# Kernel optimization log

Measured on AMD Instinct MI355X. Metric: run time of the kernel, lower is better.

Reference implementation:

```python
import jax, jax.numpy as jnp
import numpy as np

N = 50000      # nodes
E = 300000     # edges
IN = 128       # input_dim
HID = 64       # hidden_dim (per-head out_channels)
HEADS = 4
OUT = 64       # output_dim


def setup_inputs() -> dict:
    key = jax.random.key(0)
    ks = jax.random.split(key, 12)
    s_in = 1.0 / np.sqrt(IN)
    s_h = 1.0 / np.sqrt(HID)
    x = jax.random.normal(ks[0], (N, IN), jnp.float32)
    edge_index = jax.random.randint(ks[1], (2, E), 0, N, jnp.int32)
    Wq = jax.random.normal(ks[2], (IN, HEADS * HID), jnp.float32) * s_in
    bq = jax.random.normal(ks[3], (HEADS * HID,), jnp.float32) * 0.01
    Wk = jax.random.normal(ks[4], (IN, HEADS * HID), jnp.float32) * s_in
    bk = jax.random.normal(ks[5], (HEADS * HID,), jnp.float32) * 0.01
    Wv = jax.random.normal(ks[6], (IN, HEADS * HID), jnp.float32) * s_in
    bv = jax.random.normal(ks[7], (HEADS * HID,), jnp.float32) * 0.01
    Wskip = jax.random.normal(ks[8], (IN, HID), jnp.float32) * s_in
    bskip = jax.random.normal(ks[9], (HID,), jnp.float32) * 0.01
    Wmlp = jax.random.normal(ks[10], (HID, OUT), jnp.float32) * s_h  # spectral-normed, bias=False
    return {"x": x, "edge_index": edge_index, "Wq": Wq, "bq": bq, "Wk": Wk,
            "bk": bk, "Wv": Wv, "bv": bv, "Wskip": Wskip, "bskip": bskip,
            "Wmlp": Wmlp}


def _spectral_sigma(W, n_iter=20):
    # Power iteration as in torch spectral_norm; u,v detached, sigma = u^T W v.
    u = jnp.ones((W.shape[0],), W.dtype)
    u = u / jnp.linalg.norm(u)
    v = None
    for _ in range(n_iter):
        v = W.T @ u
        v = v / (jnp.linalg.norm(v) + 1e-12)
        u = W @ v
        u = u / (jnp.linalg.norm(u) + 1e-12)
    u = jax.lax.stop_gradient(u)
    v = jax.lax.stop_gradient(v)
    return u @ (W @ v)


def reference(x, edge_index, Wq, bq, Wk, bk, Wv, bv, Wskip, bskip, Wmlp):
    n = x.shape[0]
    src, dst = edge_index[0], edge_index[1]  # message flows src -> dst
    q = (x @ Wq + bq).reshape(n, HEADS, HID)
    k = (x @ Wk + bk).reshape(n, HEADS, HID)
    v = (x @ Wv + bv).reshape(n, HEADS, HID)
    # per-edge attention logits: [E, H]
    alpha = jnp.einsum('ehd,ehd->eh', q[dst], k[src]) / jnp.sqrt(jnp.float32(HID))
    # segment softmax over incoming edges of each dst node
    m = jax.ops.segment_max(alpha, dst, num_segments=n)          # [N, H]
    ex = jnp.exp(alpha - m[dst])                                  # [E, H]
    denom = jax.ops.segment_sum(ex, dst, num_segments=n)         # [N, H]
    a = ex / (denom[dst] + 1e-16)                                 # [E, H]
    msg = a[:, :, None] * v[src]                                  # [E, H, D]
    out = jax.ops.segment_sum(msg, dst, num_segments=n)          # [N, H, D]
    out = out.mean(axis=1) + x @ Wskip + bskip                    # concat=False -> head mean; root skip
    hidden = jnp.tanh(out)
    sigma = _spectral_sigma(Wmlp)
    return hidden @ (Wmlp / sigma)
```

## Files before the change

kernel.cpp:

```cpp
#include <hip/hip_runtime.h>
#include <math.h>

#define NN 50000
#define NE 300000
#define IND 128
#define QKV 256
#define QKVP 768
#define OUTD 64
#define NTOT 832
#define NCT 13
#define SCAN_B 196

typedef __attribute__((ext_vector_type(8))) short bf16x8;
typedef __attribute__((ext_vector_type(4))) float f32x4;

__device__ inline unsigned short f2bf(float f) {
    unsigned u = __float_as_uint(f);
    u = (u + 0x7FFFu + ((u >> 16) & 1u)) >> 16;
    return (unsigned short)u;
}
__device__ inline float b2f(unsigned short h) {
    return __uint_as_float(((unsigned)h) << 16);
}

__global__ __launch_bounds__(256) void pack_w(const float* __restrict__ Wq, const float* __restrict__ bq,
                                              const float* __restrict__ Wk, const float* __restrict__ bk,
                                              const float* __restrict__ Wv, const float* __restrict__ bv,
                                              const float* __restrict__ Wsk, const float* __restrict__ bsk,
                                              unsigned short* __restrict__ WT, float* __restrict__ bias) {
    int t = blockIdx.x * 256 + threadIdx.x;
    if (t >= NTOT * 128) return;
    int col = t >> 7, kk = t & 127;
    const float* W; const float* B; int c; int ld;
    if (col < 256)      { W = Wq;  B = bq;  c = col;       ld = 256; }
    else if (col < 512) { W = Wk;  B = bk;  c = col - 256; ld = 256; }
    else if (col < 768) { W = Wv;  B = bv;  c = col - 512; ld = 256; }
    else                { W = Wsk; B = bsk; c = col - 768; ld = 64;  }
    WT[t] = f2bf(W[kk * ld + c]);
    if (kk == 0) bias[col] = B[c];
}

__global__ __launch_bounds__(256) void gemm_mfma(const float* __restrict__ x,
                                                 const unsigned short* __restrict__ WT,
                                                 const float* __restrict__ bias,
                                                 unsigned short* __restrict__ qkvh,
                                                 float* __restrict__ skip) {
    __shared__ short As[64][136];
    __shared__ short Bs[64][136];
    int tid = threadIdx.x;
    int wv = tid >> 6, lane = tid & 63;
    int row0 = blockIdx.x * 64;

#pragma unroll
    for (int p = 0; p < 8; p++) {
        int idx = p * 256 + tid;
        int r = idx >> 5, c4 = (idx & 31) * 4;
        int gr = row0 + r;
        float4 v = (gr < NN) ? *(const float4*)(x + (size_t)gr * IND + c4)
                             : make_float4(0.f, 0.f, 0.f, 0.f);
        ushort4 o;
        o.x = f2bf(v.x); o.y = f2bf(v.y); o.z = f2bf(v.z); o.w = f2bf(v.w);
        *(ushort4*)(&As[r][c4]) = o;
    }

    int lr = lane & 15;
    int koff = (lane >> 4) * 8;
    int arow = wv * 16 + lr;
    int rbase = wv * 16 + ((lane >> 4) << 2);

    for (int ct = 0; ct < NCT; ct++) {
        int col0 = ct * 64;
        __syncthreads();
#pragma unroll
        for (int rr = 0; rr < 4; rr++) {
            int idx = rr * 256 + tid;
            int r = idx >> 4, c8 = (idx & 15) * 8;
            *(int4*)(&Bs[r][c8]) = *(const int4*)(WT + (size_t)(col0 + r) * 128 + c8);
        }
        __syncthreads();

        f32x4 acc[4] = {};
#pragma unroll
        for (int k0 = 0; k0 < 128; k0 += 32) {
            bf16x8 a = *(bf16x8*)(&As[arow][k0 + koff]);
#pragma unroll
            for (int cf = 0; cf < 4; cf++) {
                bf16x8 b = *(bf16x8*)(&Bs[cf * 16 + lr][k0 + koff]);
                acc[cf] = __builtin_amdgcn_mfma_f32_16x16x32_bf16(a, b, acc[cf], 0, 0, 0);
            }
        }

        if (col0 < QKVP) {
#pragma unroll
            for (int cf = 0; cf < 4; cf++) {
                int c = col0 + cf * 16 + lr; float bb = bias[c];
#pragma unroll
                for (int r = 0; r < 4; r++) {
                    int gr = row0 + rbase + r;
                    if (gr < NN) qkvh[(size_t)gr * QKVP + c] = f2bf(acc[cf][r] + bb);
                }
            }
        } else {
#pragma unroll
            for (int cf = 0; cf < 4; cf++) {
                int c = col0 + cf * 16 + lr; float bb = bias[c];
#pragma unroll
                for (int r = 0; r < 4; r++) {
                    int gr = row0 + rbase + r;
                    if (gr < NN) skip[(size_t)gr * OUTD + (c - QKVP)] = acc[cf][r] + bb;
                }
            }
        }
    }
}

__global__ void hist_dst(const int* __restrict__ ei, int* __restrict__ deg) {
    int t = blockIdx.x * blockDim.x + threadIdx.x;
    if (t < NE) atomicAdd(&deg[ei[NE + t]], 1);
}
__global__ __launch_bounds__(256) void scan1(const int* __restrict__ deg,
                                             int* __restrict__ incl, int* __restrict__ bsum) {
    __shared__ int s[256];
    int tid = threadIdx.x, i = blockIdx.x * 256 + tid;
    int v = (i < NN) ? deg[i] : 0;
    s[tid] = v; __syncthreads();
    for (int off = 1; off < 256; off <<= 1) {
        int t2 = (tid >= off) ? s[tid - off] : 0;
        __syncthreads(); s[tid] += t2; __syncthreads();
    }
    if (i < NN) incl[i] = s[tid];
    if (tid == 255) bsum[blockIdx.x] = s[255];
}
__global__ __launch_bounds__(256) void scan2(int* __restrict__ bsum, int* __restrict__ row_ptr) {
    __shared__ int s[256];
    int tid = threadIdx.x;
    int v = (tid < SCAN_B) ? bsum[tid] : 0;
    s[tid] = v; __syncthreads();
    for (int off = 1; off < 256; off <<= 1) {
        int t2 = (tid >= off) ? s[tid - off] : 0;
        __syncthreads(); s[tid] += t2; __syncthreads();
    }
    if (tid < SCAN_B) bsum[tid] = s[tid] - v;
    if (tid == 255) row_ptr[NN] = s[255];
}
__global__ __launch_bounds__(256) void scan3(const int* __restrict__ deg, const int* __restrict__ incl,
                                             const int* __restrict__ bsum,
                                             int* __restrict__ row_ptr, int* __restrict__ cursor) {
    int i = blockIdx.x * 256 + threadIdx.x;
    if (i < NN) {
        int e = incl[i] - deg[i] + bsum[blockIdx.x];
        row_ptr[i] = e; cursor[i] = e;
    }
}
__global__ void fill_csr(const int* __restrict__ ei, int* __restrict__ cursor,
                         int* __restrict__ col_src) {
    int t = blockIdx.x * blockDim.x + threadIdx.x;
    if (t < NE) {
        int pos = atomicAdd(&cursor[ei[NE + t]], 1);
        col_src[pos] = ei[t];
    }
}

__global__ __launch_bounds__(256) void fused_attn(const int* __restrict__ row_ptr,
                                                  const int* __restrict__ col_src,
                                                  const unsigned short* __restrict__ qkvh,
                                                  float* __restrict__ agg) {
    int wv = threadIdx.x >> 6;
    int lane = threadIdx.x & 63;
    int n = blockIdx.x * 4 + wv;
    if (n >= NN) return;

    ushort4 qq = *(const ushort4*)(qkvh + (size_t)n * QKVP + lane * 4);
    float4 qv = make_float4(b2f(qq.x), b2f(qq.y), b2f(qq.z), b2f(qq.w));
    float m = -1e30f, d = 0.f;
    float4 o = make_float4(0.f, 0.f, 0.f, 0.f);

    int jb = row_ptr[n], je = row_ptr[n + 1];
    for (int j = jb; j < je; j++) {
        int src = col_src[j];
        const unsigned short* srow = qkvh + (size_t)src * QKVP;
        ushort4 kq = *(const ushort4*)(srow + 256 + lane * 4);
        float s = qv.x * b2f(kq.x) + qv.y * b2f(kq.y) + qv.z * b2f(kq.z) + qv.w * b2f(kq.w);
        s += __shfl_xor(s, 1);
        s += __shfl_xor(s, 2);
        s += __shfl_xor(s, 4);
        s += __shfl_xor(s, 8);
        s *= 0.125f;
        float mn = fmaxf(m, s);
        float scale = __expf(m - mn);
        float e = __expf(s - mn);
        d = d * scale + e;
        ushort4 vq = *(const ushort4*)(srow + 512 + lane * 4);
        o.x = o.x * scale + e * b2f(vq.x);
        o.y = o.y * scale + e * b2f(vq.y);
        o.z = o.z * scale + e * b2f(vq.z);
        o.w = o.w * scale + e * b2f(vq.w);
        m = mn;
    }
    float inv = 1.0f / (d + 1e-16f);
    *(float4*)(agg + (size_t)n * QKV + lane * 4) =
        make_float4(o.x * inv, o.y * inv, o.z * inv, o.w * inv);
}

__global__ void spectral(const float* __restrict__ W, float* __restrict__ sigma) {
    __shared__ float ub[64], vb[64];
    int t = threadIdx.x;
    ub[t] = 0.125f;
    __syncthreads();
    for (int it = 0; it < 20; it++) {
        float s = 0.f;
        for (int i = 0; i < 64; i++) s += W[i * 64 + t] * ub[i];
        float ss = s * s;
        for (int off = 1; off < 64; off <<= 1) ss += __shfl_xor(ss, off);
        float vn = s / (sqrtf(ss) + 1e-12f);
        __syncthreads();
        vb[t] = vn;
        __syncthreads();
        float s2 = 0.f;
        for (int j = 0; j < 64; j++) s2 += W[t * 64 + j] * vb[j];
        float ss2 = s2 * s2;
        for (int off = 1; off < 64; off <<= 1) ss2 += __shfl_xor(ss2, off);
        ub[t] = s2 / (sqrtf(ss2) + 1e-12f);
        __syncthreads();
    }
    float wvv = 0.f;
    for (int j = 0; j < 64; j++) wvv += W[t * 64 + j] * vb[j];
    float sg = ub[t] * wvv;
    for (int off = 1; off < 64; off <<= 1) sg += __shfl_xor(sg, off);
    if (t == 0) *sigma = sg;
}

__global__ __launch_bounds__(256) void finalize(const float* __restrict__ agg,
                                                const float* __restrict__ skip,
                                                const float* __restrict__ Wmlp,
                                                const float* __restrict__ sigma,
                                                float* __restrict__ out) {
    __shared__ float Ws[64 * 64];
    __shared__ float hid[4][64];
    int tid = threadIdx.x;
    for (int i = tid; i < 64 * 64; i += 256) Ws[i] = Wmlp[i];
    float inv_sigma = 1.0f / (*sigma);
    __syncthreads();
    int wave = tid >> 6, lane = tid & 63;
    int n = blockIdx.x * 4 + wave;
    if (n < NN) {
        const float* a = agg + (size_t)n * QKV;
        float mval = 0.25f * (a[lane] + a[64 + lane] + a[128 + lane] + a[192 + lane])
                     + skip[(size_t)n * 64 + lane];
        hid[wave][lane] = tanhf(mval);
    }
    __syncthreads();
    if (n < NN) {
        float acc = 0.f;
        for (int d = 0; d < 64; d++) acc += hid[wave][d] * Ws[d * 64 + lane];
        out[(size_t)n * 64 + lane] = acc * inv_sigma;
    }
}

extern "C" void kernel_launch(void* const* d_in, const int* in_sizes, int n_in,
                              void* d_out, int out_size, void* d_ws, size_t ws_size,
                              hipStream_t stream) {
    const float* x     = (const float*)d_in[0];
    const int*   ei    = (const int*)d_in[1];
    const float* Wq    = (const float*)d_in[2];
    const float* bq    = (const float*)d_in[3];
    const float* Wk    = (const float*)d_in[4];
    const float* bk    = (const float*)d_in[5];
    const float* Wv    = (const float*)d_in[6];
    const float* bv    = (const float*)d_in[7];
    const float* Wskip = (const float*)d_in[8];
    const float* bskip = (const float*)d_in[9];
    const float* Wmlp  = (const float*)d_in[10];
    float* out = (float*)d_out;

    float* agg  = (float*)d_ws;
    float* skip = agg  + (size_t)NN * QKV;
    float* bias = skip + (size_t)NN * OUTD;
    float* sig  = bias + NTOT;
    int* deg     = (int*)(sig + 4);
    int* incl    = deg + NN;
    int* row_ptr = incl + NN;
    int* cursor  = row_ptr + NN + 4;
    int* col_src = cursor + NN;
    int* bsum    = col_src + NE;
    unsigned short* qkvh = (unsigned short*)(bsum + 256);
    unsigned short* WT   = qkvh + (size_t)NN * QKVP;

    hipLaunchKernelGGL(spectral, dim3(1), dim3(64), 0, stream, Wmlp, sig);

    hipMemsetAsync(deg, 0, NN * sizeof(int), stream);
    hipLaunchKernelGGL(hist_dst, dim3((NE + 255) / 256), dim3(256), 0, stream, ei, deg);
    hipLaunchKernelGGL(scan1, dim3(SCAN_B), dim3(256), 0, stream, deg, incl, bsum);
    hipLaunchKernelGGL(scan2, dim3(1), dim3(256), 0, stream, bsum, row_ptr);
    hipLaunchKernelGGL(scan3, dim3(SCAN_B), dim3(256), 0, stream, deg, incl, bsum, row_ptr, cursor);
    hipLaunchKernelGGL(fill_csr, dim3((NE + 255) / 256), dim3(256), 0, stream, ei, cursor, col_src);

    hipLaunchKernelGGL(pack_w, dim3((NTOT * 128 + 255) / 256), dim3(256), 0, stream,
                       Wq, bq, Wk, bk, Wv, bv, Wskip, bskip, WT, bias);

    hipLaunchKernelGGL(gemm_mfma, dim3((NN + 63) / 64), dim3(256), 0, stream,
                       x, WT, bias, qkvh, skip);

    hipLaunchKernelGGL(fused_attn, dim3((NN + 3) / 4), dim3(256), 0, stream,
                       row_ptr, col_src, qkvh, agg);

    hipLaunchKernelGGL(finalize, dim3((NN + 3) / 4), dim3(256), 0, stream,
                       agg, skip, Wmlp, sig, out);
}
```

Baseline: 318.4 us.

## Fuse finalize into attention, unroll edge loop, widen GEMM row tile

Merges the finalize stage (head mean, skip add, tanh, MLP projection) into the attention kernel, so the per-node aggregate buffer is never written to or read back from global memory. The edge loop now handles two edges per iteration with independent online-softmax states, merged at the end, to expose more memory-level parallelism on the gathers. The GEMM tile grows to 128 rows per block so each B tile load is reused twice. The spectral-norm loops are split into four partial accumulators. Costs are extra LDS and register use per block, and the Wmlp load now runs in every attention block.

```diff
diff --git a/kernel.cpp b/kernel.cpp
--- a/kernel.cpp
+++ b/kernel.cpp
@@ -45,14 +45,14 @@
                                                  const float* __restrict__ bias,
                                                  unsigned short* __restrict__ qkvh,
                                                  float* __restrict__ skip) {
-    __shared__ short As[64][136];
+    __shared__ short As[128][136];
     __shared__ short Bs[64][136];
     int tid = threadIdx.x;
     int wv = tid >> 6, lane = tid & 63;
-    int row0 = blockIdx.x * 64;
-
-#pragma unroll
-    for (int p = 0; p < 8; p++) {
+    int row0 = blockIdx.x * 128;
+
+#pragma unroll
+    for (int p = 0; p < 16; p++) {
         int idx = p * 256 + tid;
         int r = idx >> 5, c4 = (idx & 31) * 4;
         int gr = row0 + r;
@@ -65,8 +65,9 @@
 
     int lr = lane & 15;
     int koff = (lane >> 4) * 8;
-    int arow = wv * 16 + lr;
-    int rbase = wv * 16 + ((lane >> 4) << 2);
+    int arow0 = wv * 16 + lr;
+    int arow1 = 64 + arow0;
+    int rb = wv * 16 + ((lane >> 4) << 2);
 
     for (int ct = 0; ct < NCT; ct++) {
         int col0 = ct * 64;
@@ -79,35 +80,43 @@
         }
         __syncthreads();
 
-        f32x4 acc[4] = {};
+        f32x4 accA[4] = {}, accB[4] = {};
 #pragma unroll
         for (int k0 = 0; k0 < 128; k0 += 32) {
-            bf16x8 a = *(bf16x8*)(&As[arow][k0 + koff]);
+            bf16x8 a0 = *(bf16x8*)(&As[arow0][k0 + koff]);
+            bf16x8 a1 = *(bf16x8*)(&As[arow1][k0 + koff]);
 #pragma unroll
             for (int cf = 0; cf < 4; cf++) {
                 bf16x8 b = *(bf16x8*)(&Bs[cf * 16 + lr][k0 + koff]);
-                acc[cf] = __builtin_amdgcn_mfma_f32_16x16x32_bf16(a, b, acc[cf], 0, 0, 0);
+                accA[cf] = __builtin_amdgcn_mfma_f32_16x16x32_bf16(a0, b, accA[cf], 0, 0, 0);
+                accB[cf] = __builtin_amdgcn_mfma_f32_16x16x32_bf16(a1, b, accB[cf], 0, 0, 0);
             }
         }
 
-        if (col0 < QKVP) {
-#pragma unroll
-            for (int cf = 0; cf < 4; cf++) {
-                int c = col0 + cf * 16 + lr; float bb = bias[c];
-#pragma unroll
-                for (int r = 0; r < 4; r++) {
-                    int gr = row0 + rbase + r;
-                    if (gr < NN) qkvh[(size_t)gr * QKVP + c] = f2bf(acc[cf][r] + bb);
+#pragma unroll
+        for (int strip = 0; strip < 2; strip++) {
+            int gr0 = row0 + strip * 64 + rb;
+            if (col0 < QKVP) {
+#pragma unroll
+                for (int cf = 0; cf < 4; cf++) {
+                    int c = col0 + cf * 16 + lr; float bb = bias[c];
+                    f32x4 av = strip ? accB[cf] : accA[cf];
+#pragma unroll
+                    for (int r = 0; r < 4; r++) {
+                        int gr = gr0 + r;
+                        if (gr < NN) qkvh[(size_t)gr * QKVP + c] = f2bf(av[r] + bb);
+                    }
                 }
-            }
-        } else {
-#pragma unroll
-            for (int cf = 0; cf < 4; cf++) {
-                int c = col0 + cf * 16 + lr; float bb = bias[c];
-#pragma unroll
-                for (int r = 0; r < 4; r++) {
-                    int gr = row0 + rbase + r;
-                    if (gr < NN) skip[(size_t)gr * OUTD + (c - QKVP)] = acc[cf][r] + bb;
+            } else {
+#pragma unroll
+                for (int cf = 0; cf < 4; cf++) {
+                    int c = col0 + cf * 16 + lr; float bb = bias[c];
+                    f32x4 av = strip ? accB[cf] : accA[cf];
+#pragma unroll
+                    for (int r = 0; r < 4; r++) {
+                        int gr = gr0 + r;
+                        if (gr < NN) skip[(size_t)gr * OUTD + (c - QKVP)] = av[r] + bb;
+                    }
                 }
             }
         }
@@ -164,42 +173,107 @@
 __global__ __launch_bounds__(256) void fused_attn(const int* __restrict__ row_ptr,
                                                   const int* __restrict__ col_src,
                                                   const unsigned short* __restrict__ qkvh,
-                                                  float* __restrict__ agg) {
-    int wv = threadIdx.x >> 6;
-    int lane = threadIdx.x & 63;
+                                                  const float* __restrict__ skipb,
+                                                  const float* __restrict__ Wmlp,
+                                                  const float* __restrict__ sigma,
+                                                  float* __restrict__ out) {
+    __shared__ float Ws[64 * 64];
+    __shared__ float hid[4][64];
+    int tid = threadIdx.x;
+    for (int i = tid; i < 64 * 64; i += 256) Ws[i] = Wmlp[i];
+    float inv_sigma = 1.0f / (*sigma);
+    __syncthreads();
+
+    int wv = tid >> 6;
+    int lane = tid & 63;
     int n = blockIdx.x * 4 + wv;
-    if (n >= NN) return;
 
     ushort4 qq = *(const ushort4*)(qkvh + (size_t)n * QKVP + lane * 4);
     float4 qv = make_float4(b2f(qq.x), b2f(qq.y), b2f(qq.z), b2f(qq.w));
-    float m = -1e30f, d = 0.f;
-    float4 o = make_float4(0.f, 0.f, 0.f, 0.f);
+
+    float m0 = -1e30f, d0 = 0.f;
+    float4 o0 = make_float4(0.f, 0.f, 0.f, 0.f);
+    float m1 = -1e30f, d1 = 0.f;
+    float4 o1 = make_float4(0.f, 0.f, 0.f, 0.f);
 
     int jb = row_ptr[n], je = row_ptr[n + 1];
-    for (int j = jb; j < je; j++) {
-        int src = col_src[j];
-        const unsigned short* srow = qkvh + (size_t)src * QKVP;
-        ushort4 kq = *(const ushort4*)(srow + 256 + lane * 4);
-        float s = qv.x * b2f(kq.x) + qv.y * b2f(kq.y) + qv.z * b2f(kq.z) + qv.w * b2f(kq.w);
-        s += __shfl_xor(s, 1);
-        s += __shfl_xor(s, 2);
-        s += __shfl_xor(s, 4);
-        s += __shfl_xor(s, 8);
-        s *= 0.125f;
-        float mn = fmaxf(m, s);
-        float scale = __expf(m - mn);
-        float e = __expf(s - mn);
-        d = d * scale + e;
-        ushort4 vq = *(const ushort4*)(srow + 512 + lane * 4);
-        o.x = o.x * scale + e * b2f(vq.x);
-        o.y = o.y * scale + e * b2f(vq.y);
-        o.z = o.z * scale + e * b2f(vq.z);
-        o.w = o.w * scale + e * b2f(vq.w);
-        m = mn;
-    }
+    int j = jb;
+    for (; j + 1 < je; j += 2) {
+        int sA = col_src[j], sB = col_src[j + 1];
+        const unsigned short* ra = qkvh + (size_t)sA * QKVP;
+        const unsigned short* rb = qkvh + (size_t)sB * QKVP;
+        ushort4 kA = *(const ushort4*)(ra + 256 + lane * 4);
+        ushort4 kB = *(const ushort4*)(rb + 256 + lane * 4);
+        ushort4 vA = *(const ushort4*)(ra + 512 + lane * 4);
+        ushort4 vB = *(const ushort4*)(rb + 512 + lane * 4);
+        float sa = qv.x * b2f(kA.x) + qv.y * b2f(kA.y) + qv.z * b2f(kA.z) + qv.w * b2f(kA.w);
+        float sb = qv.x * b2f(kB.x) + qv.y * b2f(kB.y) + qv.z * b2f(kB.z) + qv.w * b2f(kB.w);
+        sa += __shfl_xor(sa, 1);  sb += __shfl_xor(sb, 1);
+        sa += __shfl_xor(sa, 2);  sb += __shfl_xor(sb, 2);
+        sa += __shfl_xor(sa, 4);  sb += __shfl_xor(sb, 4);
+        sa += __shfl_xor(sa, 8);  sb += __shfl_xor(sb, 8);
+        sa *= 0.125f;             sb *= 0.125f;
+        float mnA = fmaxf(m0, sa);
+        float mnB = fmaxf(m1, sb);
+        float scA = __expf(m0 - mnA), eA = __expf(sa - mnA);
+        float scB = __expf(m1 - mnB), eB = __expf(sb - mnB);
+        d0 = d0 * scA + eA;       d1 = d1 * scB + eB;
+        o0.x = o0.x * scA + eA * b2f(vA.x);  o1.x = o1.x * scB + eB * b2f(vB.x);
+        o0.y = o0.y * scA + eA * b2f(vA.y);  o1.y = o1.y * scB + eB * b2f(vB.y);
+        o0.z = o0.z * scA + eA * b2f(vA.z);  o1.z = o1.z * scB + eB * b2f(vB.z);
+        o0.w = o0.w * scA + eA * b2f(vA.w);  o1.w = o1.w * scB + eB * b2f(vB.w);
+        m0 = mnA;                 m1 = mnB;
+    }
+    if (j < je) {
+        int sA = col_src[j];
+        const unsigned short* ra = qkvh + (size_t)sA * QKVP;
+        ushort4 kA = *(const ushort4*)(ra + 256 + lane * 4);
+        ushort4 vA = *(const ushort4*)(ra + 512 + lane * 4);
+        float sa = qv.x * b2f(kA.x) + qv.y * b2f(kA.y) + qv.z * b2f(kA.z) + qv.w * b2f(kA.w);
+        sa += __shfl_xor(sa, 1);
+        sa += __shfl_xor(sa, 2);
+        sa += __shfl_xor(sa, 4);
+        sa += __shfl_xor(sa, 8);
+        sa *= 0.125f;
+        float mnA = fmaxf(m0, sa);
+        float scA = __expf(m0 - mnA), eA = __expf(sa - mnA);
+        d0 = d0 * scA + eA;
+        o0.x = o0.x * scA + eA * b2f(vA.x);
+        o0.y = o0.y * scA + eA * b2f(vA.y);
+        o0.z = o0.z * scA + eA * b2f(vA.z);
+        o0.w = o0.w * scA + eA * b2f(vA.w);
+        m0 = mnA;
+    }
+    float M = fmaxf(m0, m1);
+    float e0 = __expf(m0 - M), e1 = __expf(m1 - M);
+    float d = d0 * e0 + d1 * e1;
     float inv = 1.0f / (d + 1e-16f);
-    *(float4*)(agg + (size_t)n * QKV + lane * 4) =
-        make_float4(o.x * inv, o.y * inv, o.z * inv, o.w * inv);
+    float ox = (o0.x * e0 + o1.x * e1) * inv;
+    float oy = (o0.y * e0 + o1.y * e1) * inv;
+    float oz = (o0.z * e0 + o1.z * e1) * inv;
+    float ow = (o0.w * e0 + o1.w * e1) * inv;
+
+    ox += __shfl_xor(ox, 16); ox += __shfl_xor(ox, 32);
+    oy += __shfl_xor(oy, 16); oy += __shfl_xor(oy, 32);
+    oz += __shfl_xor(oz, 16); oz += __shfl_xor(oz, 32);
+    ow += __shfl_xor(ow, 16); ow += __shfl_xor(ow, 32);
+
+    float4 sk = *(const float4*)(skipb + (size_t)n * OUTD + (lane & 15) * 4);
+    float h0 = tanhf(0.25f * ox + sk.x);
+    float h1 = tanhf(0.25f * oy + sk.y);
+    float h2 = tanhf(0.25f * oz + sk.z);
+    float h3 = tanhf(0.25f * ow + sk.w);
+    if (lane < 16) *(float4*)(&hid[wv][lane * 4]) = make_float4(h0, h1, h2, h3);
+
+    float a0 = 0.f, a1 = 0.f, a2 = 0.f, a3 = 0.f;
+#pragma unroll
+    for (int dd = 0; dd < 64; dd += 4) {
+        a0 += hid[wv][dd + 0] * Ws[(dd + 0) * 64 + lane];
+        a1 += hid[wv][dd + 1] * Ws[(dd + 1) * 64 + lane];
+        a2 += hid[wv][dd + 2] * Ws[(dd + 2) * 64 + lane];
+        a3 += hid[wv][dd + 3] * Ws[(dd + 3) * 64 + lane];
+    }
+    out[(size_t)n * OUTD + lane] = ((a0 + a1) + (a2 + a3)) * inv_sigma;
 }
 
 __global__ void spectral(const float* __restrict__ W, float* __restrict__ sigma) {
@@ -208,53 +282,38 @@
     ub[t] = 0.125f;
     __syncthreads();
     for (int it = 0; it < 20; it++) {
-        float s = 0.f;
-        for (int i = 0; i < 64; i++) s += W[i * 64 + t] * ub[i];
+        float s0 = 0.f, s1 = 0.f, s2 = 0.f, s3 = 0.f;
+        for (int i = 0; i < 64; i += 4) {
+            s0 += W[(i + 0) * 64 + t] * ub[i + 0];
+            s1 += W[(i + 1) * 64 + t] * ub[i + 1];
+            s2 += W[(i + 2) * 64 + t] * ub[i + 2];
+            s3 += W[(i + 3) * 64 + t] * ub[i + 3];
+        }
+        float s = (s0 + s1) + (s2 + s3);
         float ss = s * s;
         for (int off = 1; off < 64; off <<= 1) ss += __shfl_xor(ss, off);
         float vn = s / (sqrtf(ss) + 1e-12f);
         __syncthreads();
         vb[t] = vn;
         __syncthreads();
-        float s2 = 0.f;
-        for (int j = 0; j < 64; j++) s2 += W[t * 64 + j] * vb[j];
-        float ss2 = s2 * s2;
+        float r0 = 0.f, r1 = 0.f, r2 = 0.f, r3 = 0.f;
+        for (int jj = 0; jj < 64; jj += 4) {
+            r0 += W[t * 64 + jj + 0] * vb[jj + 0];
+            r1 += W[t * 64 + jj + 1] * vb[jj + 1];
+            r2 += W[t * 64 + jj + 2] * vb[jj + 2];
+            r3 += W[t * 64 + jj + 3] * vb[jj + 3];
+        }
+        float s2v = (r0 + r1) + (r2 + r3);
+        float ss2 = s2v * s2v;
         for (int off = 1; off < 64; off <<= 1) ss2 += __shfl_xor(ss2, off);
-        ub[t] = s2 / (sqrtf(ss2) + 1e-12f);
-        __syncthreads();
-    }
-    float wvv = 0.f;
-    for (int j = 0; j < 64; j++) wvv += W[t * 64 + j] * vb[j];
-    float sg = ub[t] * wvv;
+        ub[t] = s2v / (sqrtf(ss2) + 1e-12f);
+        __syncthreads();
+    }
+    float w0 = 0.f;
+    for (int jj = 0; jj < 64; jj++) w0 += W[t * 64 + jj] * vb[jj];
+    float sg = ub[t] * w0;
     for (int off = 1; off < 64; off <<= 1) sg += __shfl_xor(sg, off);
     if (t == 0) *sigma = sg;
-}
-
-__global__ __launch_bounds__(256) void finalize(const float* __restrict__ agg,
-                                                const float* __restrict__ skip,
-                                                const float* __restrict__ Wmlp,
-                                                const float* __restrict__ sigma,
-                                                float* __restrict__ out) {
-    __shared__ float Ws[64 * 64];
-    __shared__ float hid[4][64];
-    int tid = threadIdx.x;
-    for (int i = tid; i < 64 * 64; i += 256) Ws[i] = Wmlp[i];
-    float inv_sigma = 1.0f / (*sigma);
-    __syncthreads();
-    int wave = tid >> 6, lane = tid & 63;
-    int n = blockIdx.x * 4 + wave;
-    if (n < NN) {
-        const float* a = agg + (size_t)n * QKV;
-        float mval = 0.25f * (a[lane] + a[64 + lane] + a[128 + lane] + a[192 + lane])
-                     + skip[(size_t)n * 64 + lane];
-        hid[wave][lane] = tanhf(mval);
-    }
-    __syncthreads();
-    if (n < NN) {
-        float acc = 0.f;
-        for (int d = 0; d < 64; d++) acc += hid[wave][d] * Ws[d * 64 + lane];
-        out[(size_t)n * 64 + lane] = acc * inv_sigma;
-    }
 }
 
 extern "C" void kernel_launch(void* const* d_in, const int* in_sizes, int n_in,
@@ -273,8 +332,7 @@
     const float* Wmlp  = (const float*)d_in[10];
     float* out = (float*)d_out;
 
-    float* agg  = (float*)d_ws;
-    float* skip = agg  + (size_t)NN * QKV;
+    float* skip = (float*)d_ws;
     float* bias = skip + (size_t)NN * OUTD;
     float* sig  = bias + NTOT;
     int* deg     = (int*)(sig + 4);
@@ -298,12 +356,9 @@
     hipLaunchKernelGGL(pack_w, dim3((NTOT * 128 + 255) / 256), dim3(256), 0, stream,
                        Wq, bq, Wk, bk, Wv, bv, Wskip, bskip, WT, bias);
 
-    hipLaunchKernelGGL(gemm_mfma, dim3((NN + 63) / 64), dim3(256), 0, stream,
+    hipLaunchKernelGGL(gemm_mfma, dim3((NN + 127) / 128), dim3(256), 0, stream,
                        x, WT, bias, qkvh, skip);
 
-    hipLaunchKernelGGL(fused_attn, dim3((NN + 3) / 4), dim3(256), 0, stream,
-                       row_ptr, col_src, qkvh, agg);
-
-    hipLaunchKernelGGL(finalize, dim3((NN + 3) / 4), dim3(256), 0, stream,
-                       agg, skip, Wmlp, sig, out);
-}
+    hipLaunchKernelGGL(fused_attn, dim3(NN / 4), dim3(256), 0, stream,
+                       row_ptr, col_src, qkvh, skip, Wmlp, sig, out);
+}
```

New measurement: 324.3 us. Within noise of the previous version (+1.9%).
